# Kernel tuning notes

Measured on AMD Instinct MI355X. Metric: run time of the kernel, lower is better.

Reference implementation:

```python
import jax, jax.numpy as jnp
import numpy as np

B = 1024      # batch
G = 2000      # num_genes
S = 32        # uniform per-gene feature width (geneid_num[i] == 32 for all i)
M1, M2, M3 = 4096, 2048, 1024  # mul_len1/2/3
H = 64        # hidden width of all small MLPs


def setup_inputs() -> dict:
    key = jax.random.key(0)
    ks = jax.random.split(key, 24)
    n = lambda k, shape, s=0.02: jax.random.normal(k, shape, dtype=jnp.float32) * s
    return {
        # activations
        "x":  jax.random.normal(ks[0], (B, G * S), dtype=jnp.float32),
        "z1": jax.random.normal(ks[1], (B, M1), dtype=jnp.float32),
        "z2": jax.random.normal(ks[2], (B, M2), dtype=jnp.float32),
        "z3": jax.random.normal(ks[3], (B, M3), dtype=jnp.float32),
        # per-gene Linear(S,1) weights, stacked: block-diagonal gene stage
        "Wg": n(ks[4], (G, S)), "bg": n(ks[5], (G,)),
        # fc0: Linear(G, 64); fc1/2/3: Linear(Mi, 64). Layout (in, out).
        "W0": n(ks[6], (G, H)),  "b0": n(ks[7], (H,)),
        "W1": n(ks[8], (M1, H)), "b1": n(ks[9], (H,)),
        "W2": n(ks[10], (M2, H)), "b2": n(ks[11], (H,)),
        "W3": n(ks[12], (M3, H)), "b3": n(ks[13], (H,)),
        # learned fusion weights (init 0.5 in torch)
        "w1": jnp.full((H,), 0.5, jnp.float32),
        "w2": jnp.full((H,), 0.5, jnp.float32),
        "w3": jnp.full((H,), 0.5, jnp.float32),
        # final fc: 64->64->64->1
        "fW1": n(ks[14], (H, H)), "fb1": n(ks[15], (H,)),
        "fW2": n(ks[16], (H, H)), "fb2": n(ks[17], (H,)),
        "fW3": n(ks[18], (H, 1)), "fb3": n(ks[19], (1,)),
    }


def reference(x, z1, z2, z3, Wg, bg, W0, b0, W1, b1, W2, b2, W3, b3,
              w1, w2, w3, fW1, fb1, fW2, fb2, fW3, fb3):
    g, s = Wg.shape
    b = x.shape[0]
    # ragged per-gene Linear(numi,1)+ReLU loop == block-diagonal contraction
    # x: [B, G*S] -> [B, G, S]; gene_outputs: [B, G]
    gene = jax.nn.relu(jnp.einsum('bgs,gs->bg', x.reshape(b, g, s), Wg) + bg)
    h0 = jax.nn.relu(gene @ W0 + b0)                 # fc0(gene_outputs)  [B, 64]
    d1 = jax.nn.relu(z1 @ W1 + b1) * w1 + h0         # fc1(z1)*weights_1 + fc0
    d2 = jax.nn.relu(z2 @ W2 + b2) * w2 + d1         # fc2(z2)*weights_2 + d1
    d3 = jax.nn.relu(z3 @ W3 + b3) * w3 + d2         # fc3(z3)*weights_3 + d2
    h = jax.nn.relu(d3 @ fW1 + fb1)
    h = jax.nn.relu(h @ fW2 + fb2)
    return h @ fW3 + fb3                             # [B, 1]
```

## Files before the change

### kernel.cpp

```cpp
#include <hip/hip_runtime.h>

constexpr int BB = 1024;
constexpr int GG = 2000;
constexpr int SS = 32;
constexpr int K1 = 4096, K2 = 2048, K3 = 1024;

constexpr int BH = BB * 64;

constexpr int Y1P_OFF = 0;
constexpr int Y2P_OFF = 4 * BH;
constexpr int Y3P_OFF = 6 * BH;
constexpr int HP_OFF  = 7 * BH;

constexpr int NCH       = 63;
constexpr int RPB       = 16;
constexpr int NGENE_BLK = NCH * (BB / RPB);
constexpr int NGEMM_BLK = 224;
constexpr int KCH       = 1024;

__global__ __launch_bounds__(256, 8) void k1_gene_fc0_zgemm(
    const float* __restrict__ x,  const float* __restrict__ z1,
    const float* __restrict__ z2, const float* __restrict__ z3,
    const float* __restrict__ Wg, const float* __restrict__ bg,
    const float* __restrict__ W0,
    const float* __restrict__ W1, const float* __restrict__ W2,
    const float* __restrict__ W3, float* __restrict__ ws)
{
    __shared__ float lds[4608];
    const int bid = blockIdx.x;
    const int t   = threadIdx.x;

    if (bid >= NGEMM_BLK) {
        const int gid   = bid - NGEMM_BLK;
        const int chunk = gid % NCH;
        const int bgrp  = gid / NCH;
        const int g0    = chunk * 32;
        const int b0    = bgrp * RPB;
        const int gene  = t >> 3;
        const int sub   = t & 7;
        const int g     = g0 + gene;
        const bool gv   = (g < GG);

        float4 wg4 = make_float4(0.f, 0.f, 0.f, 0.f);
        if (gv) wg4 = ((const float4*)Wg)[g * 8 + sub];

        const float* xp = gv ? (x + (size_t)b0 * (GG * SS) + (size_t)g * SS + sub * 4)
                             : x;

        float* part = lds;
        float* gS   = lds + 4096;

        #pragma unroll
        for (int ii = 0; ii < RPB; ii += 8) {
            float4 xr[8];
            #pragma unroll
            for (int j = 0; j < 8; ++j)
                xr[j] = *(const float4*)(xp + (size_t)(ii + j) * (GG * SS));
            #pragma unroll
            for (int j = 0; j < 8; ++j) {
                float p = (xr[j].x * wg4.x + xr[j].y * wg4.y)
                        + (xr[j].z * wg4.z + xr[j].w * wg4.w);
                part[(ii + j) * 256 + t] = p;
            }
        }
        __syncthreads();

        #pragma unroll
        for (int p = t; p < RPB * 32; p += 256) {
            const float4 a = *(const float4*)&part[p * 8];
            const float4 b = *(const float4*)&part[p * 8 + 4];
            float s = ((a.x + a.y) + (a.z + a.w)) + ((b.x + b.y) + (b.z + b.w));
            const int gg = g0 + (p & 31);
            const float bias = (gg < GG) ? bg[gg] : 0.f;
            gS[p] = fmaxf(s + bias, 0.f);
        }
        __syncthreads();

        const int n = t & 63;
        const int w = t >> 6;
        float acc0 = 0.f, acc1 = 0.f, acc2 = 0.f, acc3 = 0.f;
        const float* gSw = gS + (w * 4) * 32;
        #pragma unroll 8
        for (int j = 0; j < 32; ++j) {
            int gj = g0 + j; if (gj >= GG) gj = GG - 1;
            const float w0v = W0[(size_t)gj * 64 + n];
            acc0 = fmaf(gSw[j],      w0v, acc0);
            acc1 = fmaf(gSw[32 + j], w0v, acc1);
            acc2 = fmaf(gSw[64 + j], w0v, acc2);
            acc3 = fmaf(gSw[96 + j], w0v, acc3);
        }
        float* hp = ws + HP_OFF + (size_t)chunk * BH + (size_t)b0 * 64;
        hp[(size_t)(w * 4 + 0) * 64 + n] = acc0;
        hp[(size_t)(w * 4 + 1) * 64 + n] = acc1;
        hp[(size_t)(w * 4 + 2) * 64 + n] = acc2;
        hp[(size_t)(w * 4 + 3) * 64 + n] = acc3;
    } else {
        const int id = bid;
        const float* z; const float* W; int K; int mt; int kslab; float* ys;
        if (id < 128)      { z = z1; W = W1; K = K1; mt = id >> 2; kslab = id & 3;
                             ys = ws + Y1P_OFF + (size_t)kslab * BH; }
        else if (id < 192) { int l = id - 128; z = z2; W = W2; K = K2; mt = l >> 1; kslab = l & 1;
                             ys = ws + Y2P_OFF + (size_t)kslab * BH; }
        else               { int l = id - 192; z = z3; W = W3; K = K3; mt = l; kslab = 0;
                             ys = ws + Y3P_OFF; }

        const int m0    = mt * 32;
        const int kbase = kslab * KCH;
        const int n2    = t & 31;
        const int mq    = t >> 5;
        float* zt = lds;
        float* wt = lds + 32 * 36;

        float2 acc[4];
        #pragma unroll
        for (int j = 0; j < 4; ++j) acc[j] = make_float2(0.f, 0.f);

        const int zr = t >> 3, zc = (t & 7) * 4;
        for (int kc = 0; kc < KCH / 32; ++kc) {
            const int k0 = kbase + kc * 32;
            *(float4*)&zt[zr * 36 + zc] =
                *(const float4*)&z[(size_t)(m0 + zr) * K + k0 + zc];
            #pragma unroll
            for (int r = 0; r < 2; ++r) {
                const int idx = t + r * 256;
                const int row = idx >> 4;
                const int c4  = (idx & 15) * 4;
                *(float4*)&wt[row * 68 + c4] =
                    *(const float4*)&W[(size_t)(k0 + row) * 64 + c4];
            }
            __syncthreads();
            #pragma unroll
            for (int kk = 0; kk < 32; kk += 4) {
                const float2 wv0 = *(const float2*)&wt[(kk + 0) * 68 + n2 * 2];
                const float2 wv1 = *(const float2*)&wt[(kk + 1) * 68 + n2 * 2];
                const float2 wv2 = *(const float2*)&wt[(kk + 2) * 68 + n2 * 2];
                const float2 wv3 = *(const float2*)&wt[(kk + 3) * 68 + n2 * 2];
                #pragma unroll
                for (int j = 0; j < 4; ++j) {
                    const float4 zj = *(const float4*)&zt[(mq * 4 + j) * 36 + kk];
                    acc[j].x = fmaf(zj.x, wv0.x, acc[j].x); acc[j].y = fmaf(zj.x, wv0.y, acc[j].y);
                    acc[j].x = fmaf(zj.y, wv1.x, acc[j].x); acc[j].y = fmaf(zj.y, wv1.y, acc[j].y);
                    acc[j].x = fmaf(zj.z, wv2.x, acc[j].x); acc[j].y = fmaf(zj.z, wv2.y, acc[j].y);
                    acc[j].x = fmaf(zj.w, wv3.x, acc[j].x); acc[j].y = fmaf(zj.w, wv3.y, acc[j].y);
                }
            }
            __syncthreads();
        }
        #pragma unroll
        for (int j = 0; j < 4; ++j)
            *(float2*)&ys[(size_t)(m0 + mq * 4 + j) * 64 + n2 * 2] = acc[j];
    }
}

__global__ __launch_bounds__(256, 4) void k2_combine_mlp(
    const float* __restrict__ ws,
    const float* __restrict__ b0v,
    const float* __restrict__ b1v, const float* __restrict__ b2v,
    const float* __restrict__ b3v,
    const float* __restrict__ w1v, const float* __restrict__ w2v,
    const float* __restrict__ w3v,
    const float* __restrict__ fW1, const float* __restrict__ fb1,
    const float* __restrict__ fW2, const float* __restrict__ fb2,
    const float* __restrict__ fW3, const float* __restrict__ fb3,
    float* __restrict__ out)
{
    const float* Y1p = ws + Y1P_OFF;
    const float* Y2p = ws + Y2P_OFF;
    const float* Y3p = ws + Y3P_OFF;

    const int t   = threadIdx.x;
    const int n   = t & 63;
    const int w   = t >> 6;
    const int row = blockIdx.x * 4 + w;
    const int rn  = row * 64 + n;

    float h = 0.f;
    const float* hp = ws + HP_OFF + rn;
    #pragma unroll 9
    for (int c = 0; c < NCH; ++c) h += hp[(size_t)c * BH];
    const float h0 = fmaxf(h + b0v[n], 0.f);

    const float y1 = Y1p[rn] + Y1p[BH + rn] + Y1p[2 * BH + rn] + Y1p[3 * BH + rn];
    float d = fmaf(fmaxf(y1 + b1v[n], 0.f), w1v[n], h0);
    const float y2 = Y2p[rn] + Y2p[BH + rn];
    d = fmaf(fmaxf(y2 + b2v[n], 0.f), w2v[n], d);
    const float y3 = Y3p[rn];
    d = fmaf(fmaxf(y3 + b3v[n], 0.f), w3v[n], d);

    __shared__ float sd[4][64];
    __shared__ float sh[4][64];
    sd[w][n] = d;
    __syncthreads();
    float a1 = fb1[n];
    #pragma unroll 8
    for (int j = 0; j < 64; ++j) a1 = fmaf(sd[w][j], fW1[j * 64 + n], a1);
    a1 = fmaxf(a1, 0.f);
    sh[w][n] = a1;
    __syncthreads();
    float a2 = fb2[n];
    #pragma unroll 8
    for (int j = 0; j < 64; ++j) a2 = fmaf(sh[w][j], fW2[j * 64 + n], a2);
    a2 = fmaxf(a2, 0.f);

    float v = a2 * fW3[n];
    #pragma unroll
    for (int o = 32; o > 0; o >>= 1) v += __shfl_xor(v, o);
    if (n == 0) out[row] = v + fb3[0];
}

extern "C" void kernel_launch(void* const* d_in, const int* in_sizes, int n_in,
                              void* d_out, int out_size, void* d_ws, size_t ws_size,
                              hipStream_t stream)
{
    const float* x   = (const float*)d_in[0];
    const float* z1  = (const float*)d_in[1];
    const float* z2  = (const float*)d_in[2];
    const float* z3  = (const float*)d_in[3];
    const float* Wg  = (const float*)d_in[4];
    const float* bg  = (const float*)d_in[5];
    const float* W0  = (const float*)d_in[6];
    const float* b0v = (const float*)d_in[7];
    const float* W1  = (const float*)d_in[8];
    const float* b1v = (const float*)d_in[9];
    const float* W2  = (const float*)d_in[10];
    const float* b2v = (const float*)d_in[11];
    const float* W3  = (const float*)d_in[12];
    const float* b3v = (const float*)d_in[13];
    const float* w1v = (const float*)d_in[14];
    const float* w2v = (const float*)d_in[15];
    const float* w3v = (const float*)d_in[16];
    const float* fW1 = (const float*)d_in[17];
    const float* fb1 = (const float*)d_in[18];
    const float* fW2 = (const float*)d_in[19];
    const float* fb2 = (const float*)d_in[20];
    const float* fW3 = (const float*)d_in[21];
    const float* fb3 = (const float*)d_in[22];

    float* ws  = (float*)d_ws;
    float* out = (float*)d_out;

    k1_gene_fc0_zgemm<<<dim3(NGEMM_BLK + NGENE_BLK), dim3(256), 0, stream>>>(
        x, z1, z2, z3, Wg, bg, W0, W1, W2, W3, ws);

    k2_combine_mlp<<<dim3(BB / 4), dim3(256), 0, stream>>>(
        ws, b0v, b1v, b2v, b3v, w1v, w2v, w3v,
        fW1, fb1, fW2, fb2, fW3, fb3, out);
}
```

Before: 436.6 us.

## Split fc0 out of gene stage into separate tiled GEMM kernel

The gene stage now has each thread compute one gene's full 32-wide dot product for 8 batch rows and write relu outputs to a padded gene buffer. It no longer computes per-chunk fc0 partials that later needed a 63-way reduction. A new kernel runs fc0 as an LDS-tiled GEMM over 4 K-slabs, and the combine kernel sums only 4 partials. This cuts partial-sum traffic and the scattered W0 reads, at the cost of an extra launch and a round trip of the gene buffer through memory. Per-thread 128-byte x reads are strided across threads, which may hurt coalescing.

```diff
diff --git a/kernel.cpp b/kernel.cpp
--- a/kernel.cpp
+++ b/kernel.cpp
@@ -4,6 +4,8 @@
 constexpr int GG = 2000;
 constexpr int SS = 32;
 constexpr int K1 = 4096, K2 = 2048, K3 = 1024;
+constexpr int XROW = GG * SS;
+constexpr int GPAD = 2048;
 
 constexpr int BH = BB * 64;
 
@@ -11,89 +13,64 @@
 constexpr int Y2P_OFF = 4 * BH;
 constexpr int Y3P_OFF = 6 * BH;
 constexpr int HP_OFF  = 7 * BH;
-
-constexpr int NCH       = 63;
-constexpr int RPB       = 16;
-constexpr int NGENE_BLK = NCH * (BB / RPB);
+constexpr int GP_OFF  = 11 * BH;
+
 constexpr int NGEMM_BLK = 224;
+constexpr int NGENE_BLK = 1024;
 constexpr int KCH       = 1024;
 
-__global__ __launch_bounds__(256, 8) void k1_gene_fc0_zgemm(
+__global__ __launch_bounds__(256, 4) void k1_gene_zgemm(
     const float* __restrict__ x,  const float* __restrict__ z1,
     const float* __restrict__ z2, const float* __restrict__ z3,
     const float* __restrict__ Wg, const float* __restrict__ bg,
-    const float* __restrict__ W0,
     const float* __restrict__ W1, const float* __restrict__ W2,
     const float* __restrict__ W3, float* __restrict__ ws)
 {
-    __shared__ float lds[4608];
+    __shared__ float lds[32 * 36 + 32 * 68];
     const int bid = blockIdx.x;
     const int t   = threadIdx.x;
 
     if (bid >= NGEMM_BLK) {
-        const int gid   = bid - NGEMM_BLK;
-        const int chunk = gid % NCH;
-        const int bgrp  = gid / NCH;
-        const int g0    = chunk * 32;
-        const int b0    = bgrp * RPB;
-        const int gene  = t >> 3;
-        const int sub   = t & 7;
-        const int g     = g0 + gene;
-        const bool gv   = (g < GG);
-
-        float4 wg4 = make_float4(0.f, 0.f, 0.f, 0.f);
-        if (gv) wg4 = ((const float4*)Wg)[g * 8 + sub];
-
-        const float* xp = gv ? (x + (size_t)b0 * (GG * SS) + (size_t)g * SS + sub * 4)
-                             : x;
-
-        float* part = lds;
-        float* gS   = lds + 4096;
-
-        #pragma unroll
-        for (int ii = 0; ii < RPB; ii += 8) {
-            float4 xr[8];
-            #pragma unroll
-            for (int j = 0; j < 8; ++j)
-                xr[j] = *(const float4*)(xp + (size_t)(ii + j) * (GG * SS));
-            #pragma unroll
-            for (int j = 0; j < 8; ++j) {
-                float p = (xr[j].x * wg4.x + xr[j].y * wg4.y)
-                        + (xr[j].z * wg4.z + xr[j].w * wg4.w);
-                part[(ii + j) * 256 + t] = p;
-            }
-        }
-        __syncthreads();
-
-        #pragma unroll
-        for (int p = t; p < RPB * 32; p += 256) {
-            const float4 a = *(const float4*)&part[p * 8];
-            const float4 b = *(const float4*)&part[p * 8 + 4];
-            float s = ((a.x + a.y) + (a.z + a.w)) + ((b.x + b.y) + (b.z + b.w));
-            const int gg = g0 + (p & 31);
-            const float bias = (gg < GG) ? bg[gg] : 0.f;
-            gS[p] = fmaxf(s + bias, 0.f);
-        }
-        __syncthreads();
-
-        const int n = t & 63;
-        const int w = t >> 6;
-        float acc0 = 0.f, acc1 = 0.f, acc2 = 0.f, acc3 = 0.f;
-        const float* gSw = gS + (w * 4) * 32;
-        #pragma unroll 8
-        for (int j = 0; j < 32; ++j) {
-            int gj = g0 + j; if (gj >= GG) gj = GG - 1;
-            const float w0v = W0[(size_t)gj * 64 + n];
-            acc0 = fmaf(gSw[j],      w0v, acc0);
-            acc1 = fmaf(gSw[32 + j], w0v, acc1);
-            acc2 = fmaf(gSw[64 + j], w0v, acc2);
-            acc3 = fmaf(gSw[96 + j], w0v, acc3);
-        }
-        float* hp = ws + HP_OFF + (size_t)chunk * BH + (size_t)b0 * 64;
-        hp[(size_t)(w * 4 + 0) * 64 + n] = acc0;
-        hp[(size_t)(w * 4 + 1) * 64 + n] = acc1;
-        hp[(size_t)(w * 4 + 2) * 64 + n] = acc2;
-        hp[(size_t)(w * 4 + 3) * 64 + n] = acc3;
+        const int gid = bid - NGEMM_BLK;
+        const int sg  = gid >> 7;
+        const int rb  = gid & 127;
+        const int g   = sg * 256 + t;
+        const bool gv = (g < GG);
+        const int gcl = gv ? g : 0;
+
+        float4 wg[8];
+        #pragma unroll
+        for (int c = 0; c < 8; ++c)
+            wg[c] = *(const float4*)(Wg + (size_t)gcl * SS + c * 4);
+        const float bias = bg[gcl];
+
+        const float* xp = x + (size_t)(rb * 8) * XROW + (size_t)gcl * SS;
+        float* gp = ws + GP_OFF + (size_t)(rb * 8) * GPAD + sg * 256 + t;
+
+        #pragma unroll
+        for (int it = 0; it < 4; ++it) {
+            const float* pa = xp + (size_t)(it * 2) * XROW;
+            const float* pb = pa + XROW;
+            float4 xa[8], xb[8];
+            #pragma unroll
+            for (int c = 0; c < 8; ++c) xa[c] = *(const float4*)(pa + c * 4);
+            #pragma unroll
+            for (int c = 0; c < 8; ++c) xb[c] = *(const float4*)(pb + c * 4);
+
+            float ax = 0.f, ay = 0.f, az = 0.f, aw = 0.f;
+            float bx = 0.f, by = 0.f, bz = 0.f, bw = 0.f;
+            #pragma unroll
+            for (int c = 0; c < 8; ++c) {
+                ax = fmaf(xa[c].x, wg[c].x, ax); ay = fmaf(xa[c].y, wg[c].y, ay);
+                az = fmaf(xa[c].z, wg[c].z, az); aw = fmaf(xa[c].w, wg[c].w, aw);
+                bx = fmaf(xb[c].x, wg[c].x, bx); by = fmaf(xb[c].y, wg[c].y, by);
+                bz = fmaf(xb[c].z, wg[c].z, bz); bw = fmaf(xb[c].w, wg[c].w, bw);
+            }
+            const float sa = (ax + ay) + (az + aw);
+            const float sb = (bx + by) + (bz + bw);
+            gp[(size_t)(it * 2) * GPAD]     = gv ? fmaxf(sa + bias, 0.f) : 0.f;
+            gp[(size_t)(it * 2 + 1) * GPAD] = gv ? fmaxf(sb + bias, 0.f) : 0.f;
+        }
     } else {
         const int id = bid;
         const float* z; const float* W; int K; int mt; int kslab; float* ys;
@@ -152,7 +129,67 @@
     }
 }
 
-__global__ __launch_bounds__(256, 4) void k2_combine_mlp(
+__global__ __launch_bounds__(256, 4) void k2_fc0_gemm(
+    const float* __restrict__ ws_c, const float* __restrict__ W0,
+    float* __restrict__ ws)
+{
+    __shared__ float lds[32 * 36 + 32 * 68];
+    const int t  = threadIdx.x;
+    const int mt  = blockIdx.x >> 2;
+    const int ksl = blockIdx.x & 3;
+    const int m0    = mt * 32;
+    const int kbase = ksl * 512;
+
+    const float* gene = ws_c + GP_OFF;
+    float* hp = ws + HP_OFF + (size_t)ksl * BH;
+
+    const int n2 = t & 31;
+    const int mq = t >> 5;
+    float* zt = lds;
+    float* wt = lds + 32 * 36;
+
+    float2 acc[4];
+    #pragma unroll
+    for (int j = 0; j < 4; ++j) acc[j] = make_float2(0.f, 0.f);
+
+    const int zr = t >> 3, zc = (t & 7) * 4;
+    for (int kc = 0; kc < 16; ++kc) {
+        const int k0 = kbase + kc * 32;
+        *(float4*)&zt[zr * 36 + zc] =
+            *(const float4*)&gene[(size_t)(m0 + zr) * GPAD + k0 + zc];
+        #pragma unroll
+        for (int r = 0; r < 2; ++r) {
+            const int idx = t + r * 256;
+            const int row = idx >> 4;
+            const int c4  = (idx & 15) * 4;
+            int krow = k0 + row; if (krow >= GG) krow = GG - 1;
+            *(float4*)&wt[row * 68 + c4] =
+                *(const float4*)&W0[(size_t)krow * 64 + c4];
+        }
+        __syncthreads();
+        #pragma unroll
+        for (int kk = 0; kk < 32; kk += 4) {
+            const float2 wv0 = *(const float2*)&wt[(kk + 0) * 68 + n2 * 2];
+            const float2 wv1 = *(const float2*)&wt[(kk + 1) * 68 + n2 * 2];
+            const float2 wv2 = *(const float2*)&wt[(kk + 2) * 68 + n2 * 2];
+            const float2 wv3 = *(const float2*)&wt[(kk + 3) * 68 + n2 * 2];
+            #pragma unroll
+            for (int j = 0; j < 4; ++j) {
+                const float4 zj = *(const float4*)&zt[(mq * 4 + j) * 36 + kk];
+                acc[j].x = fmaf(zj.x, wv0.x, acc[j].x); acc[j].y = fmaf(zj.x, wv0.y, acc[j].y);
+                acc[j].x = fmaf(zj.y, wv1.x, acc[j].x); acc[j].y = fmaf(zj.y, wv1.y, acc[j].y);
+                acc[j].x = fmaf(zj.z, wv2.x, acc[j].x); acc[j].y = fmaf(zj.z, wv2.y, acc[j].y);
+                acc[j].x = fmaf(zj.w, wv3.x, acc[j].x); acc[j].y = fmaf(zj.w, wv3.y, acc[j].y);
+            }
+        }
+        __syncthreads();
+    }
+    #pragma unroll
+    for (int j = 0; j < 4; ++j)
+        *(float2*)&hp[(size_t)(m0 + mq * 4 + j) * 64 + n2 * 2] = acc[j];
+}
+
+__global__ __launch_bounds__(256, 4) void k3_combine_mlp(
     const float* __restrict__ ws,
     const float* __restrict__ b0v,
     const float* __restrict__ b1v, const float* __restrict__ b2v,
@@ -167,6 +204,7 @@
     const float* Y1p = ws + Y1P_OFF;
     const float* Y2p = ws + Y2P_OFF;
     const float* Y3p = ws + Y3P_OFF;
+    const float* Hp  = ws + HP_OFF;
 
     const int t   = threadIdx.x;
     const int n   = t & 63;
@@ -174,10 +212,7 @@
     const int row = blockIdx.x * 4 + w;
     const int rn  = row * 64 + n;
 
-    float h = 0.f;
-    const float* hp = ws + HP_OFF + rn;
-    #pragma unroll 9
-    for (int c = 0; c < NCH; ++c) h += hp[(size_t)c * BH];
+    const float h = Hp[rn] + Hp[BH + rn] + Hp[2 * BH + rn] + Hp[3 * BH + rn];
     const float h0 = fmaxf(h + b0v[n], 0.f);
 
     const float y1 = Y1p[rn] + Y1p[BH + rn] + Y1p[2 * BH + rn] + Y1p[3 * BH + rn];
@@ -239,10 +274,12 @@
     float* ws  = (float*)d_ws;
     float* out = (float*)d_out;
 
-    k1_gene_fc0_zgemm<<<dim3(NGEMM_BLK + NGENE_BLK), dim3(256), 0, stream>>>(
-        x, z1, z2, z3, Wg, bg, W0, W1, W2, W3, ws);
-
-    k2_combine_mlp<<<dim3(BB / 4), dim3(256), 0, stream>>>(
+    k1_gene_zgemm<<<dim3(NGEMM_BLK + NGENE_BLK), dim3(256), 0, stream>>>(
+        x, z1, z2, z3, Wg, bg, W1, W2, W3, ws);
+
+    k2_fc0_gemm<<<dim3(128), dim3(256), 0, stream>>>(ws, W0, ws);
+
+    k3_combine_mlp<<<dim3(BB / 4), dim3(256), 0, stream>>>(
         ws, b0v, b1v, b2v, b3v, w1v, w2v, w3v,
         fW1, fb1, fW2, fb2, fW3, fb3, out);
 }
```

After: 468.8 us. 7.4% more time.
